# Performance work log

Measured on AMD Instinct MI355X. Metric: run time of the kernel, lower is better.

## Reference

```python
import jax, jax.numpy as jnp
import numpy as np

B = 131072
N_CAT = 29
VOCABS = np.array([2,2,2,2,2,3,3,4,4,4,3,3,3,4,4,4,4,4,4,4,2,2,2,2,2,2,2,2,2], dtype=np.int32)
MAX_V = 4
EPS = 1e-5


def setup_inputs():
    key = jax.random.key(0)
    ks = jax.random.split(key, 24)
    # input: [B, 36] = 7 continuous + 29 categorical (stored as float, cast in forward)
    xcon = jax.random.normal(ks[0], (B, 7), jnp.float32)
    raw = jax.random.randint(ks[1], (B, N_CAT), 0, 10_000)
    xcat = (raw % jnp.asarray(VOCABS)[None, :]).astype(jnp.float32)  # in-range per column
    x = jnp.concatenate([xcon, xcat], axis=1)
    s = 0.2
    # stacked per-feature branch params (embedding tables padded to MAX_V rows)
    E  = jax.random.normal(ks[2], (N_CAT, MAX_V, 12), jnp.float32)
    W1 = jax.random.normal(ks[3], (N_CAT, 12, 12), jnp.float32) * s
    b1 = jax.random.normal(ks[4], (N_CAT, 12), jnp.float32) * s
    W2 = jax.random.normal(ks[5], (N_CAT, 12), jnp.float32) * s
    b2 = jax.random.normal(ks[6], (N_CAT,), jnp.float32) * s
    rW1 = jax.random.normal(ks[7], (36, 768), jnp.float32) * s
    rb1 = jax.random.normal(ks[8], (768,), jnp.float32) * s
    g1  = jax.random.normal(ks[9], (768,), jnp.float32) * 0.1 + 1.0
    be1 = jax.random.normal(ks[10], (768,), jnp.float32) * 0.1
    m1  = jax.random.normal(ks[11], (768,), jnp.float32) * 0.1
    v1  = jnp.abs(jax.random.normal(ks[12], (768,), jnp.float32)) * 0.1 + 1.0
    rW2 = jax.random.normal(ks[13], (768, 64), jnp.float32) * (s / 4)
    rb2 = jax.random.normal(ks[14], (64,), jnp.float32) * s
    g2  = jax.random.normal(ks[15], (64,), jnp.float32) * 0.1 + 1.0
    be2 = jax.random.normal(ks[16], (64,), jnp.float32) * 0.1
    m2  = jax.random.normal(ks[17], (64,), jnp.float32) * 0.1
    v2  = jnp.abs(jax.random.normal(ks[18], (64,), jnp.float32)) * 0.1 + 1.0
    rW3 = jax.random.normal(ks[19], (64, 16), jnp.float32) * s
    rb3 = jax.random.normal(ks[20], (16,), jnp.float32) * s
    rW4 = jax.random.normal(ks[21], (16, 1), jnp.float32) * s
    rb4 = jax.random.normal(ks[22], (1,), jnp.float32) * s
    return dict(x=x, E=E, W1=W1, b1=b1, W2=W2, b2=b2,
                rW1=rW1, rb1=rb1, g1=g1, be1=be1, m1=m1, v1=v1,
                rW2=rW2, rb2=rb2, g2=g2, be2=be2, m2=m2, v2=v2,
                rW3=rW3, rb3=rb3, rW4=rW4, rb4=rb4)


def _forward(x, E, W1, b1, W2, b2, rW1, rb1, g1, be1, m1, v1,
             rW2, rb2, g2, be2, m2, v2, rW3, rb3, rW4, rb4):
    xcon = x[:, :7]
    idx = jax.lax.stop_gradient(x[:, 7:]).astype(jnp.int32)          # [B, 29]
    # batched gather: one embedding row per (sample, feature)
    emb = E[jnp.arange(N_CAT)[None, :], idx]                          # [B, 29, 12]
    h = jax.nn.relu(jnp.einsum('bfd,fde->bfe', emb, W1) + b1[None])   # [B, 29, 12]
    o = jax.nn.relu(jnp.einsum('bfd,fd->bf', h, W2) + b2[None])       # [B, 29]
    xin = jnp.concatenate([xcon, o], axis=1)                          # [B, 36]
    # head (BatchNorm eval mode, Dropout = identity)
    h1 = xin @ rW1 + rb1
    h1 = jax.nn.relu((h1 - m1) * jax.lax.rsqrt(v1 + EPS) * g1 + be1)
    h2 = h1 @ rW2 + rb2
    h2 = jax.nn.relu((h2 - m2) * jax.lax.rsqrt(v2 + EPS) * g2 + be2)
    h3 = jax.nn.relu(h2 @ rW3 + rb3)
    out = jax.nn.sigmoid(h3 @ rW4 + rb4)                              # [B, 1]
    return out


def reference(x, E, W1, b1, W2, b2, rW1, rb1, g1, be1, m1, v1,
              rW2, rb2, g2, be2, m2, v2, rW3, rb3, rW4, rb4):
    return _forward(x, E, W1, b1, W2, b2, rW1, rb1, g1, be1, m1, v1,
                    rW2, rb2, g2, be2, m2, v2, rW3, rb3, rW4, rb4)
```

## Files before the change

### kernel.cpp

```cpp
#include <hip/hip_runtime.h>
#include <math.h>

typedef _Float16 half8 __attribute__((ext_vector_type(8)));
typedef float floatx16 __attribute__((ext_vector_type(16)));
typedef unsigned int uintx4 __attribute__((ext_vector_type(4)));
typedef unsigned int uintx2 __attribute__((ext_vector_type(2)));

#define EPSV 1e-5f

#define CHUNK_BYTES 14336
#define OFF_TILES 0
#define OFF_W3    (12 * CHUNK_BYTES)
#define OFF_T2    (OFF_W3 + 4096)
#define OFF_OTAB  (OFF_T2 + 256)

__device__ __forceinline__ unsigned pk2(float a, float b) {
  _Float16 ha = (_Float16)a, hb = (_Float16)b;
  return (unsigned)__builtin_bit_cast(unsigned short, ha) |
         ((unsigned)__builtin_bit_cast(unsigned short, hb) << 16);
}
__device__ __forceinline__ void plswap(unsigned &a, unsigned &b) {
  uintx2 r = __builtin_amdgcn_permlane32_swap(a, b, false, false);
  a = r[0];
  b = r[1];
}
__device__ __forceinline__ half8 mk_bfrag(float v0, float v1, float v2, float v3,
                                          float v4, float v5, float v6, float v7) {
  unsigned r0 = pk2(fmaxf(v0, 0.f), fmaxf(v1, 0.f));
  unsigned r1 = pk2(fmaxf(v2, 0.f), fmaxf(v3, 0.f));
  unsigned r2 = pk2(fmaxf(v4, 0.f), fmaxf(v5, 0.f));
  unsigned r3 = pk2(fmaxf(v6, 0.f), fmaxf(v7, 0.f));
  plswap(r0, r2);
  plswap(r1, r3);
  uintx4 uv = {r0, r1, r2, r3};
  return __builtin_bit_cast(half8, uv);
}
__device__ __forceinline__ floatx16 zero16() {
  floatx16 z;
  #pragma unroll
  for (int i = 0; i < 16; ++i) z[i] = 0.f;
  return z;
}

__global__ void prep_kernel(const float* __restrict__ E,  const float* __restrict__ W1,
                            const float* __restrict__ b1, const float* __restrict__ W2,
                            const float* __restrict__ b2,
                            const float* __restrict__ rW1, const float* __restrict__ rb1,
                            const float* __restrict__ g1,  const float* __restrict__ be1,
                            const float* __restrict__ m1,  const float* __restrict__ v1,
                            const float* __restrict__ rW2, const float* __restrict__ rb2,
                            const float* __restrict__ g2,  const float* __restrict__ be2,
                            const float* __restrict__ m2,  const float* __restrict__ v2,
                            const float* __restrict__ rW3, char* __restrict__ ws)
{
  _Float16* tiles = (_Float16*)(ws + OFF_TILES);
  _Float16* w3t   = (_Float16*)(ws + OFF_W3);
  float*    t2o   = (float*)(ws + OFF_T2);
  float*    otab  = (float*)(ws + OFF_OTAB);

  const int NTI = 12 * 7168;
  const int NW3 = 2048;
  const int NT2 = 64;
  const int NOT = 116;
  const int NT  = NTI + NW3 + NT2 + NOT;

  for (int i = blockIdx.x * blockDim.x + threadIdx.x; i < NT; i += gridDim.x * blockDim.x) {
    int j = i;
    if (j < NTI) {
      const int ct = j / 7168;
      const int e  = j - ct * 7168;
      if (e < 3072) {
        const int f  = e >> 9, li = (e >> 3) & 63, el = e & 7;
        const int nt = f / 3, ks = f - nt * 3;
        const int n  = ct * 64 + nt * 32 + (li & 31);
        const int k  = ks * 16 + (li >> 5) * 8 + el;
        float val = 0.f;
        const float S1 = g1[n] * rsqrtf(v1[n] + EPSV);
        if (k < 36)       val = rW1[(size_t)k * 768 + n] * S1;
        else if (k == 36) val = (rb1[n] - m1[n]) * S1 + be1[n];
        tiles[j] = (_Float16)val;
      } else {
        const int e2 = e - 3072;
        const int f  = e2 >> 9, li = (e2 >> 3) & 63, el = e2 & 7;
        const int n2t = f >> 2, kc = f & 3;
        const int n2 = n2t * 32 + (li & 31);
        const int k  = ct * 64 + kc * 16 + (li >> 5) * 8 + el;
        const float S2 = g2[n2] * rsqrtf(v2[n2] + EPSV);
        tiles[j] = (_Float16)(rW2[(size_t)k * 64 + n2] * S2);
      }
      continue;
    }
    j -= NTI;
    if (j < NW3) {
      const int f3 = j >> 9, li = (j >> 3) & 63, el = j & 7;
      const int n3 = li & 31;
      const int k  = f3 * 16 + (li >> 5) * 8 + el;
      w3t[j] = (n3 < 16) ? (_Float16)rW3[(size_t)k * 16 + n3] : (_Float16)0.f;
      continue;
    }
    j -= NW3;
    if (j < NT2) {
      const float S2 = g2[j] * rsqrtf(v2[j] + EPSV);
      t2o[j] = (rb2[j] - m2[j]) * S2 + be2[j];
      continue;
    }
    j -= NT2;
    {
      const int f = j >> 2, v = j & 3;
      const float* ev  = E + ((f << 2) + v) * 12;
      const float* w1f = W1 + f * 144;
      float emb[12];
      #pragma unroll
      for (int d = 0; d < 12; ++d) emb[d] = ev[d];
      float acc_o = b2[f];
      #pragma unroll
      for (int ee = 0; ee < 12; ++ee) {
        float h = b1[f * 12 + ee];
        #pragma unroll
        for (int d = 0; d < 12; ++d) h = fmaf(emb[d], w1f[d * 12 + ee], h);
        h = fmaxf(h, 0.f);
        acc_o = fmaf(h, W2[f * 12 + ee], acc_o);
      }
      otab[f * 4 + v] = fmaxf(acc_o, 0.f);
    }
  }
}

__device__ __forceinline__ float feat_val(const float* xv, const float* otab, int c) {
  if (c < 7)  return xv[c];
  if (c < 36) return otab[(c - 7) * 4 + (int)xv[c]];
  if (c == 36) return 1.0f;
  return 0.f;
}

__global__ __launch_bounds__(256, 3)
void fused_mfma_kernel(const float* __restrict__ x,
                       const float* __restrict__ rb3,
                       const float* __restrict__ rW4,
                       const float* __restrict__ rb4,
                       const char* __restrict__ ws,
                       float* __restrict__ out)
{
  const int t  = threadIdx.x;
  const int w  = t >> 6;
  const int l  = t & 63;
  const int lm = l & 31;
  const int hi = l >> 5;

  const int nwg = gridDim.x;
  const int bid = (blockIdx.x & 7) * (nwg >> 3) + (blockIdx.x >> 3);
  const int b0 = bid * 128;
  const int row = b0 + w * 32 + lm;

  unsigned wbits[24];
  {
    const float* xr = x + (size_t)row * 36;
    float xv[36];
    #pragma unroll
    for (int i = 0; i < 9; ++i) {
      float4 v = *(const float4*)(xr + 4 * i);
      xv[4 * i + 0] = v.x; xv[4 * i + 1] = v.y;
      xv[4 * i + 2] = v.z; xv[4 * i + 3] = v.w;
    }
    const float* otab = (const float*)(ws + OFF_OTAB);
    #pragma unroll
    for (int c2 = 0; c2 < 19; ++c2)
      wbits[c2] = pk2(feat_val(xv, otab, 2 * c2), feat_val(xv, otab, 2 * c2 + 1));
    #pragma unroll
    for (int c2 = 19; c2 < 24; ++c2) wbits[c2] = 0u;
  }

  half8 xf[3];
  #pragma unroll
  for (int ks = 0; ks < 3; ++ks) {
    unsigned wq[4];
    #pragma unroll
    for (int q = 0; q < 4; ++q)
      wq[q] = hi ? wbits[ks * 8 + 4 + q] : wbits[ks * 8 + q];
    uintx4 u = {wq[0], wq[1], wq[2], wq[3]};
    xf[ks] = __builtin_bit_cast(half8, u);
  }

  const char* wsl = ws + (size_t)l * 16;

  floatx16 acc0 = zero16(), acc1 = zero16();

  #pragma unroll
  for (int ct = 0; ct < 12; ++ct) {
    const char* src = wsl + (size_t)ct * CHUNK_BYTES;
    half8 w1c[6], w2c[8];
    #pragma unroll
    for (int f = 0; f < 6; ++f)
      w1c[f] = *(const half8*)(src + f * 1024);
    #pragma unroll
    for (int f = 0; f < 8; ++f)
      w2c[f] = *(const half8*)(src + 6144 + f * 1024);

    __builtin_amdgcn_s_setprio(1);
    #pragma unroll
    for (int nt = 0; nt < 2; ++nt) {
      floatx16 c1m = zero16();
      #pragma unroll
      for (int ks = 0; ks < 3; ++ks)
        c1m = __builtin_amdgcn_mfma_f32_32x32x16_f16(w1c[nt * 3 + ks], xf[ks], c1m, 0, 0, 0);
      #pragma unroll
      for (int hf = 0; hf < 2; ++hf) {
        const int kc = nt * 2 + hf;
        const int b = hf * 8;
        half8 bf = mk_bfrag(c1m[b+0], c1m[b+1], c1m[b+2], c1m[b+3],
                            c1m[b+4], c1m[b+5], c1m[b+6], c1m[b+7]);
        acc0 = __builtin_amdgcn_mfma_f32_32x32x16_f16(w2c[0 * 4 + kc], bf, acc0, 0, 0, 0);
        acc1 = __builtin_amdgcn_mfma_f32_32x32x16_f16(w2c[1 * 4 + kc], bf, acc1, 0, 0, 0);
      }
    }
    __builtin_amdgcn_s_setprio(0);
  }

  const float* T2p = (const float*)(ws + OFF_T2);
  const _Float16* gW3 = (const _Float16*)(ws + OFF_W3);
  floatx16 c3 = zero16();

  #pragma unroll
  for (int n2t = 0; n2t < 2; ++n2t) {
    const floatx16 am = n2t ? acc1 : acc0;
    float h0[16];
    #pragma unroll
    for (int r = 0; r < 16; ++r) {
      const float t2v = T2p[n2t * 32 + (r & 3) + 8 * (r >> 2) + 4 * hi];
      h0[r] = fmaxf(am[r] + t2v, 0.f);
    }
    #pragma unroll
    for (int hf = 0; hf < 2; ++hf) {
      const int kc = n2t * 2 + hf;
      const int b = hf * 8;
      half8 bf = mk_bfrag(h0[b+0], h0[b+1], h0[b+2], h0[b+3],
                          h0[b+4], h0[b+5], h0[b+6], h0[b+7]);
      half8 a3 = *(const half8*)&gW3[(kc * 64 + l) * 8];
      c3 = __builtin_amdgcn_mfma_f32_32x32x16_f16(a3, bf, c3, 0, 0, 0);
    }
  }
  {
    float s0 = 0.f;
    const float bb = rb4[0];
    #pragma unroll
    for (int r = 0; r < 8; ++r) {
      const int n3 = (r & 3) + 8 * (r >> 2) + 4 * hi;
      s0 += fmaxf(c3[r] + rb3[n3], 0.f) * rW4[n3];
    }
    s0 += __shfl_xor(s0, 32, 64);
    if (hi == 0)
      out[row] = 1.f / (1.f + expf(-(s0 + bb)));
  }
}

extern "C" void kernel_launch(void* const* d_in, const int* in_sizes, int n_in,
                              void* d_out, int out_size, void* d_ws, size_t ws_size,
                              hipStream_t stream) {
  const float* x   = (const float*)d_in[0];
  const float* E   = (const float*)d_in[1];
  const float* W1  = (const float*)d_in[2];
  const float* b1  = (const float*)d_in[3];
  const float* W2  = (const float*)d_in[4];
  const float* b2  = (const float*)d_in[5];
  const float* rW1 = (const float*)d_in[6];
  const float* rb1 = (const float*)d_in[7];
  const float* g1  = (const float*)d_in[8];
  const float* be1 = (const float*)d_in[9];
  const float* m1  = (const float*)d_in[10];
  const float* v1  = (const float*)d_in[11];
  const float* rW2 = (const float*)d_in[12];
  const float* rb2 = (const float*)d_in[13];
  const float* g2  = (const float*)d_in[14];
  const float* be2 = (const float*)d_in[15];
  const float* m2  = (const float*)d_in[16];
  const float* v2  = (const float*)d_in[17];
  const float* rW3 = (const float*)d_in[18];
  const float* rb3 = (const float*)d_in[19];
  const float* rW4 = (const float*)d_in[20];
  const float* rb4 = (const float*)d_in[21];
  float* out = (float*)d_out;
  char* ws = (char*)d_ws;

  prep_kernel<<<128, 256, 0, stream>>>(E, W1, b1, W2, b2,
                                       rW1, rb1, g1, be1, m1, v1,
                                       rW2, rb2, g2, be2, m2, v2,
                                       rW3, ws);

  const int B = in_sizes[0] / 36;
  dim3 grid(B / 128), block(256);
  fused_mfma_kernel<<<grid, block, 0, stream>>>(x, rb3, rW4, rb4, ws, out);
}
```

Baseline: 40.04 us.

## Stage weight chunks into double-buffered LDS with async global-to-LDS loads

Weight tiles for each of the 12 chunks are now copied cooperatively into a double-buffered shared-memory area with global_load_lds, and the next chunk is prefetched while the current one is consumed. Each wave then reads its fragments from LDS instead of every wave fetching the same data from global memory. The two layer-1 MFMA chains are also interleaved so they run independently. The cost is 28KB of LDS per block and a barrier per chunk, which may limit occupancy at 3 blocks per CU. Only a __syncthreads orders the async LDS writes before they are read, with no explicit vmcnt wait.

Measured after the change: 38.11 us. 4.8% less time.

```diff
diff --git a/kernel.cpp b/kernel.cpp
--- a/kernel.cpp
+++ b/kernel.cpp
@@ -13,6 +13,9 @@
 #define OFF_W3    (12 * CHUNK_BYTES)
 #define OFF_T2    (OFF_W3 + 4096)
 #define OFF_OTAB  (OFF_T2 + 256)
+
+typedef __attribute__((address_space(3))) char      lds_char;
+typedef __attribute__((address_space(3))) unsigned  lds_uint;
 
 __device__ __forceinline__ unsigned pk2(float a, float b) {
   _Float16 ha = (_Float16)a, hb = (_Float16)b;
@@ -133,6 +136,19 @@
   return 0.f;
 }
 
+__device__ __forceinline__ void stage_chunk(const char* gsrc, lds_char* ldst, int w, int l) {
+  #pragma unroll
+  for (int i = 0; i < 4; ++i) {
+    const int f = w + 4 * i;
+    if (f < 14) {
+      __builtin_amdgcn_global_load_lds(
+          (const __attribute__((address_space(1))) unsigned int*)(gsrc + f * 1024 + (size_t)l * 16),
+          (lds_uint*)(ldst + f * 1024),
+          16, 0, 0);
+    }
+  }
+}
+
 __global__ __launch_bounds__(256, 3)
 void fused_mfma_kernel(const float* __restrict__ x,
                        const float* __restrict__ rb3,
@@ -152,6 +168,13 @@
   const int b0 = bid * 128;
   const int row = b0 + w * 32 + lm;
 
+  __shared__ __align__(16) char smem[2 * CHUNK_BYTES];
+  lds_char* lds0 = (lds_char*)smem;
+
+  const char* tiles = ws + OFF_TILES;
+
+  stage_chunk(tiles, lds0, w, l);
+
   unsigned wbits[24];
   {
     const float* xr = x + (size_t)row * 36;
@@ -181,28 +204,37 @@
     xf[ks] = __builtin_bit_cast(half8, u);
   }
 
-  const char* wsl = ws + (size_t)l * 16;
+  __syncthreads();
 
   floatx16 acc0 = zero16(), acc1 = zero16();
 
   #pragma unroll
   for (int ct = 0; ct < 12; ++ct) {
-    const char* src = wsl + (size_t)ct * CHUNK_BYTES;
+    const char* cbuf = smem + (ct & 1) * CHUNK_BYTES;
+
+    if (ct < 11)
+      stage_chunk(tiles + (size_t)(ct + 1) * CHUNK_BYTES,
+                  lds0 + ((ct + 1) & 1) * CHUNK_BYTES, w, l);
+
+    const char* srcl = cbuf + (size_t)l * 16;
     half8 w1c[6], w2c[8];
     #pragma unroll
     for (int f = 0; f < 6; ++f)
-      w1c[f] = *(const half8*)(src + f * 1024);
+      w1c[f] = *(const half8*)(srcl + f * 1024);
     #pragma unroll
     for (int f = 0; f < 8; ++f)
-      w2c[f] = *(const half8*)(src + 6144 + f * 1024);
+      w2c[f] = *(const half8*)(srcl + 6144 + f * 1024);
 
     __builtin_amdgcn_s_setprio(1);
+    floatx16 p0 = zero16(), p1 = zero16();
+    #pragma unroll
+    for (int ks = 0; ks < 3; ++ks) {
+      p0 = __builtin_amdgcn_mfma_f32_32x32x16_f16(w1c[ks],     xf[ks], p0, 0, 0, 0);
+      p1 = __builtin_amdgcn_mfma_f32_32x32x16_f16(w1c[3 + ks], xf[ks], p1, 0, 0, 0);
+    }
     #pragma unroll
     for (int nt = 0; nt < 2; ++nt) {
-      floatx16 c1m = zero16();
-      #pragma unroll
-      for (int ks = 0; ks < 3; ++ks)
-        c1m = __builtin_amdgcn_mfma_f32_32x32x16_f16(w1c[nt * 3 + ks], xf[ks], c1m, 0, 0, 0);
+      const floatx16 c1m = nt ? p1 : p0;
       #pragma unroll
       for (int hf = 0; hf < 2; ++hf) {
         const int kc = nt * 2 + hf;
@@ -214,6 +246,9 @@
       }
     }
     __builtin_amdgcn_s_setprio(0);
+
+    if (ct < 11)
+      __syncthreads();
   }
 
   const float* T2p = (const float*)(ws + OFF_T2);
```
